# Kernel tuning notes

Measured on AMD Instinct MI355X. Metric: run time of the kernel, lower is better.

The kernel has to match this reference:

```python
import jax, jax.numpy as jnp
import numpy as np

B, T, E, H = 8, 2048, 512, 16
D = E // H  # 32 embeddings per head
LN_EPS = 1e-3  # keras LayerNormalization default epsilon
DECAY = 1.2


def setup_inputs() -> dict:
    key = jax.random.key(0)
    k0, k1, k2 = jax.random.split(key, 3)
    x = jax.random.normal(k0, (B, T, E), dtype=jnp.float32)
    W = jax.random.normal(k1, (E, E), dtype=jnp.float32) * (1.0 / np.sqrt(E))
    b = jnp.zeros((E,), dtype=jnp.float32)
    concept_map = jax.random.normal(k2, (H, D, D, D), dtype=jnp.float32) * 0.02
    gamma = jnp.ones((E,), dtype=jnp.float32)
    beta = jnp.zeros((E,), dtype=jnp.float32)
    return {"x": x, "W": W, "b": b, "concept_map": concept_map,
            "gamma": gamma, "beta": beta}


def reference(x, W, b, concept_map, gamma, beta):
    Bn, Tn, En = x.shape
    Hn = concept_map.shape[0]
    Dn = En // Hn
    # Dense projection, split into heads: (B,T,H,D)
    h = (jnp.einsum('bte,ef->btf', x, W) + b).reshape(Bn, Tn, Hn, Dn)
    # Decayed cumulative sum of preceding tokens: S_0 = 0, S_t = (S_{t-1} + h_{t-1}) / 1.2
    def step(s, h_t):
        return (s + h_t) / DECAY, s
    _, S = jax.lax.scan(step, jnp.zeros((Bn, Hn, Dn), h.dtype),
                        jnp.swapaxes(h, 0, 1))  # S: (T,B,H,D)
    S = jnp.swapaxes(S, 0, 1)  # (B,T,H,D)
    # Fused bilinear contraction: sum_{i,j} h[...,i] * S[...,j] * C[h,k,i,j]
    # (equivalent to outer-product * concept_map then reduce_sum over last two dims)
    y = jnp.einsum('bthi,bthj,hkij->bthk', h, S, concept_map) + h
    y = y.reshape(Bn, Tn, En)
    # LayerNormalization over last axis (keras default eps=1e-3)
    mu = jnp.mean(y, axis=-1, keepdims=True)
    var = jnp.var(y, axis=-1, keepdims=True)
    y = (y - mu) * jax.lax.rsqrt(var + LN_EPS) * gamma + beta
    # Dropout: identity at inference
    return y
```

## Files before the change

### kernel.cpp

```cpp
#include <hip/hip_runtime.h>
#include <hip/hip_bf16.h>

#define Bn 8
#define Tn 2048
#define En 512
#define Hn 16
#define Dn 32
#define NC 32
#define CL 64
#define NT (Bn*Tn)
#define INV_DECAY (1.0f/1.2f)

typedef __attribute__((ext_vector_type(8))) short  bf16x8;
typedef __attribute__((ext_vector_type(4))) float  f32x4;
typedef __attribute__((ext_vector_type(8))) unsigned short u16x8;

__device__ __forceinline__ unsigned short f2b(float f) {
    __hip_bfloat16 h = __float2bfloat16(f);
    return *reinterpret_cast<unsigned short*>(&h);
}
__device__ __forceinline__ float b2f(unsigned short u) {
    union { unsigned int i; float f; } c; c.i = ((unsigned int)u) << 16; return c.f;
}

__device__ __forceinline__ size_t hm(int hd, int tok, int ch) {
    return (size_t)hd * ((size_t)NT * Dn) + (size_t)tok * Dn + ch;
}

__global__ __launch_bounds__(256) void prep_k(const float* __restrict__ C,
                                              unsigned short* __restrict__ Cl,
                                              const float* __restrict__ W,
                                              unsigned short* __restrict__ Wt) {
    __shared__ float tile[32][33];
    if (blockIdx.x < 256) {
        const int g = blockIdx.x * 256 + threadIdx.x;
        const int hd = g >> 12, rem = g & 4095;
        const int i = rem >> 7, half = (rem >> 6) & 1, lane = rem & 63;
        const int tloc = lane & 15, kgrp = lane >> 4;
        const int k = half * 16 + tloc;
        const float* src = C + (size_t)hd * 32768 + (size_t)k * 1024 + i * 32 + kgrp * 8;
        float4 a = reinterpret_cast<const float4*>(src)[0];
        float4 b = reinterpret_cast<const float4*>(src)[1];
        u16x8 st;
        st[0]=f2b(a.x); st[1]=f2b(a.y); st[2]=f2b(a.z); st[3]=f2b(a.w);
        st[4]=f2b(b.x); st[5]=f2b(b.y); st[6]=f2b(b.z); st[7]=f2b(b.w);
        *reinterpret_cast<u16x8*>(Cl + (size_t)g * 8) = st;
    } else {
        const int bid = blockIdx.x - 256;
        const int kb = (bid & 15) * 32, nb = (bid >> 4) * 32;
        const int tx = threadIdx.x & 31, ty = threadIdx.x >> 5;
        #pragma unroll
        for (int j = 0; j < 4; j++)
            tile[ty + 8 * j][tx] = W[(size_t)(kb + ty + 8 * j) * En + nb + tx];
        __syncthreads();
        #pragma unroll
        for (int j = 0; j < 4; j++)
            Wt[(size_t)(nb + ty + 8 * j) * En + kb + tx] = f2b(tile[tx][ty + 8 * j]);
    }
}

__global__ __launch_bounds__(256) void gemm_mfma_k(const float* __restrict__ x,
                                                   const unsigned short* __restrict__ Wt,
                                                   const float* __restrict__ bias,
                                                   unsigned short* __restrict__ h) {
    __shared__ unsigned short As[128][40];
    __shared__ unsigned short Bs[64][40];
    const int m0 = blockIdx.x * 128, n0 = blockIdx.y * 64;
    const int tid = threadIdx.x;
    const int wid = tid >> 6, lane = tid & 63;
    const int tloc = lane & 15, kgrp = lane >> 4;
    const int wr = wid >> 1, wc = wid & 1;

    const int ar = tid >> 1, ah = (tid & 1) * 16;
    const int brr = tid >> 2, bq = (tid & 3) * 8;

    f32x4 acc[4][2] = {};

    for (int k0 = 0; k0 < En; k0 += 32) {
        const float* xp = &x[(size_t)(m0 + ar) * En + k0 + ah];
        float4 a0 = reinterpret_cast<const float4*>(xp)[0];
        float4 a1 = reinterpret_cast<const float4*>(xp)[1];
        float4 a2 = reinterpret_cast<const float4*>(xp)[2];
        float4 a3 = reinterpret_cast<const float4*>(xp)[3];
        u16x8 bv = *reinterpret_cast<const u16x8*>(&Wt[(size_t)(n0 + brr) * En + k0 + bq]);
        __syncthreads();
        u16x8 w0, w1;
        w0[0]=f2b(a0.x); w0[1]=f2b(a0.y); w0[2]=f2b(a0.z); w0[3]=f2b(a0.w);
        w0[4]=f2b(a1.x); w0[5]=f2b(a1.y); w0[6]=f2b(a1.z); w0[7]=f2b(a1.w);
        w1[0]=f2b(a2.x); w1[1]=f2b(a2.y); w1[2]=f2b(a2.z); w1[3]=f2b(a2.w);
        w1[4]=f2b(a3.x); w1[5]=f2b(a3.y); w1[6]=f2b(a3.z); w1[7]=f2b(a3.w);
        *reinterpret_cast<u16x8*>(&As[ar][ah])     = w0;
        *reinterpret_cast<u16x8*>(&As[ar][ah + 8]) = w1;
        *reinterpret_cast<u16x8*>(&Bs[brr][bq])    = bv;
        __syncthreads();

        bf16x8 afr[4], bfr[2];
        #pragma unroll
        for (int m = 0; m < 4; m++)
            afr[m] = *reinterpret_cast<const bf16x8*>(&As[wr * 64 + m * 16 + tloc][kgrp * 8]);
        #pragma unroll
        for (int n = 0; n < 2; n++)
            bfr[n] = *reinterpret_cast<const bf16x8*>(&Bs[wc * 32 + n * 16 + tloc][kgrp * 8]);
        #pragma unroll
        for (int m = 0; m < 4; m++)
            #pragma unroll
            for (int n = 0; n < 2; n++)
                acc[m][n] = __builtin_amdgcn_mfma_f32_16x16x32_bf16(afr[m], bfr[n], acc[m][n], 0, 0, 0);
    }

    #pragma unroll
    for (int n = 0; n < 2; n++) {
        const int col = n0 + wc * 32 + n * 16 + tloc;
        const float bcol = bias[col];
        const int hd = col >> 5, ch = col & 31;
        #pragma unroll
        for (int m = 0; m < 4; m++)
            #pragma unroll
            for (int r = 0; r < 4; r++) {
                const int row = m0 + wr * 64 + m * 16 + kgrp * 4 + r;
                h[hm(hd, row, ch)] = f2b(acc[m][n][r] + bcol);
            }
    }
}

__global__ __launch_bounds__(512) void scan_local_k(const unsigned short* __restrict__ h,
                                                    float* __restrict__ locals) {
    const int c = blockIdx.x, b = blockIdx.y;
    const int e = threadIdx.x;
    const int hd = e >> 5, ch = e & 31;
    const unsigned short* hp = h + hm(hd, b * Tn + c * CL, ch);
    float s = 0.f;
    for (int t = 0; t < CL; t++) s = (s + b2f(hp[(size_t)t * Dn])) * INV_DECAY;
    locals[(size_t)(b * NC + c) * En + e] = s;
}

__global__ __launch_bounds__(512) void scan_prefix_k(const float* __restrict__ locals,
                                                     float* __restrict__ Acar) {
    const int b = blockIdx.x;
    const int e = threadIdx.x;
    float invRL = 1.f;
    #pragma unroll
    for (int i = 0; i < CL; i++) invRL *= INV_DECAY;
    float A = 0.f;
    for (int c = 0; c < NC; c++) {
        Acar[(size_t)(b * NC + c) * En + e] = A;
        A = A * invRL + locals[(size_t)(b * NC + c) * En + e];
    }
}

__global__ __launch_bounds__(512) void scan_emit_k(const unsigned short* __restrict__ h,
                                                   const float* __restrict__ Acar,
                                                   unsigned short* __restrict__ Sg) {
    const int c = blockIdx.x, b = blockIdx.y;
    const int e = threadIdx.x;
    const int hd = e >> 5, ch = e & 31;
    float s = Acar[(size_t)(b * NC + c) * En + e];
    const size_t base = hm(hd, b * Tn + c * CL, ch);
    for (int t = 0; t < CL; t++) {
        Sg[base + (size_t)t * Dn] = f2b(s);
        s = (s + b2f(h[base + (size_t)t * Dn])) * INV_DECAY;
    }
}

__global__ __launch_bounds__(256) void bilinear7_k(const unsigned short* __restrict__ hg,
                                                   unsigned short* __restrict__ Sio,
                                                   const unsigned short* __restrict__ Cl) {
    __shared__ float ys[4][64][34];

    const int hd = blockIdx.y;
    const int tid = threadIdx.x;
    const int wid = tid >> 6, lane = tid & 63;
    const int tloc = lane & 15, kgrp = lane >> 4;
    const int j0 = kgrp * 8;
    const int tokens0 = blockIdx.x * 256 + wid * 64;

    u16x8 hreg[4][4];
    float sf[4][8];
    #pragma unroll
    for (int m = 0; m < 4; m++) {
        const int trow = tokens0 + m * 16 + tloc;
        const unsigned short* hrow = hg + hm(hd, trow, 0);
        #pragma unroll
        for (int q = 0; q < 4; q++)
            hreg[m][q] = *reinterpret_cast<const u16x8*>(hrow + q * 8);
        u16x8 sv = *reinterpret_cast<const u16x8*>(Sio + hm(hd, trow, j0));
        #pragma unroll
        for (int e = 0; e < 8; e++) sf[m][e] = b2f(sv[e]);
    }

    f32x4 acc[4][2] = {};
    const bf16x8* bb = reinterpret_cast<const bf16x8*>(Cl + (size_t)hd * 32768);

    #pragma unroll
    for (int i = 0; i < Dn; i++) {
        bf16x8 b0 = bb[i * 128 + lane];
        bf16x8 b1 = bb[i * 128 + 64 + lane];
        #pragma unroll
        for (int m = 0; m < 4; m++) {
            const float hsc = b2f(hreg[m][i >> 3][i & 7]);
            bf16x8 a;
            #pragma unroll
            for (int e = 0; e < 8; e++) a[e] = (short)f2b(hsc * sf[m][e]);
            acc[m][0] = __builtin_amdgcn_mfma_f32_16x16x32_bf16(a, b0, acc[m][0], 0, 0, 0);
            acc[m][1] = __builtin_amdgcn_mfma_f32_16x16x32_bf16(a, b1, acc[m][1], 0, 0, 0);
        }
    }

    #pragma unroll
    for (int m = 0; m < 4; m++)
        #pragma unroll
        for (int nt = 0; nt < 2; nt++)
            #pragma unroll
            for (int r = 0; r < 4; r++)
                ys[wid][m * 16 + kgrp * 4 + r][nt * 16 + tloc] = acc[m][nt][r];
    __syncthreads();

    {
        const float* yrow = &ys[wid][lane][0];
        const unsigned short* hrow = hg + hm(hd, tokens0 + lane, 0);
        unsigned short* orow = Sio + hm(hd, tokens0 + lane, 0);
        #pragma unroll
        for (int q = 0; q < 4; q++) {
            u16x8 hres = *reinterpret_cast<const u16x8*>(hrow + q * 8);
            u16x8 s;
            #pragma unroll
            for (int e2 = 0; e2 < 4; e2++) {
                float2 v = *reinterpret_cast<const float2*>(yrow + q * 8 + e2 * 2);
                s[e2 * 2]     = f2b(v.x + b2f(hres[e2 * 2]));
                s[e2 * 2 + 1] = f2b(v.y + b2f(hres[e2 * 2 + 1]));
            }
            *reinterpret_cast<u16x8*>(orow + q * 8) = s;
        }
    }
}

__global__ __launch_bounds__(256) void ln_k(const unsigned short* __restrict__ y,
                                            const float* __restrict__ gamma,
                                            const float* __restrict__ beta,
                                            float* __restrict__ out) {
    const int row = blockIdx.x * 4 + (threadIdx.x >> 6);
    const int lane = threadIdx.x & 63;
    u16x8 v = *reinterpret_cast<const u16x8*>(y + hm(lane >> 2, row, (lane & 3) * 8));
    float f[8];
    float s = 0.f, s2 = 0.f;
    #pragma unroll
    for (int e = 0; e < 8; e++) {
        f[e] = b2f(v[e]);
        s += f[e]; s2 += f[e] * f[e];
    }
    #pragma unroll
    for (int off = 1; off < 64; off <<= 1) {
        s  += __shfl_xor(s, off);
        s2 += __shfl_xor(s2, off);
    }
    const float mu = s * (1.f / En);
    const float var = s2 * (1.f / En) - mu * mu;
    const float rs = rsqrtf(var + 1e-3f);
    const int cbase = lane * 8;
    float4 g0 = reinterpret_cast<const float4*>(&gamma[cbase])[0];
    float4 g1 = reinterpret_cast<const float4*>(&gamma[cbase])[1];
    float4 b0 = reinterpret_cast<const float4*>(&beta[cbase])[0];
    float4 b1 = reinterpret_cast<const float4*>(&beta[cbase])[1];
    float4 o0, o1;
    o0.x = (f[0] - mu) * rs * g0.x + b0.x; o0.y = (f[1] - mu) * rs * g0.y + b0.y;
    o0.z = (f[2] - mu) * rs * g0.z + b0.z; o0.w = (f[3] - mu) * rs * g0.w + b0.w;
    o1.x = (f[4] - mu) * rs * g1.x + b1.x; o1.y = (f[5] - mu) * rs * g1.y + b1.y;
    o1.z = (f[6] - mu) * rs * g1.z + b1.z; o1.w = (f[7] - mu) * rs * g1.w + b1.w;
    float* op = out + (size_t)row * En;
    reinterpret_cast<float4*>(op)[lane * 2]     = o0;
    reinterpret_cast<float4*>(op)[lane * 2 + 1] = o1;
}

extern "C" void kernel_launch(void* const* d_in, const int* in_sizes, int n_in,
                              void* d_out, int out_size, void* d_ws, size_t ws_size,
                              hipStream_t stream) {
    const float* x     = (const float*)d_in[0];
    const float* W     = (const float*)d_in[1];
    const float* bias  = (const float*)d_in[2];
    const float* C     = (const float*)d_in[3];
    const float* gamma = (const float*)d_in[4];
    const float* beta  = (const float*)d_in[5];
    float* out = (float*)d_out;

    unsigned short* hb  = (unsigned short*)d_ws;
    unsigned short* Sg  = hb + (size_t)Hn * NT * Dn;
    unsigned short* Cl  = Sg + (size_t)Hn * NT * Dn;
    unsigned short* Wt  = Cl + (size_t)Hn * Dn * Dn * Dn;
    float* locals = (float*)(Wt + (size_t)En * En);
    float* Acar   = locals + (size_t)Bn * NC * En;

    prep_k<<<512, 256, 0, stream>>>(C, Cl, W, Wt);
    gemm_mfma_k<<<dim3(NT / 128, En / 64), 256, 0, stream>>>(x, Wt, bias, hb);
    scan_local_k<<<dim3(NC, Bn), 512, 0, stream>>>(hb, locals);
    scan_prefix_k<<<Bn, 512, 0, stream>>>(locals, Acar);
    scan_emit_k<<<dim3(NC, Bn), 512, 0, stream>>>(hb, Acar, Sg);
    bilinear7_k<<<dim3(NT / 256, Hn), 256, 0, stream>>>(hb, Sg, Cl);
    ln_k<<<NT / 4, 256, 0, stream>>>(Sg, gamma, beta, out);
}
```

Baseline: 91.37 us.

## Split bilinear contraction over i across waves with register-resident concept-map fragments

The bilinear kernel now gives each wave a quarter of the i dimension and keeps that slice of the concept map in registers as MFMA A operands, instead of streaming the whole concept map per wave for 64 tokens. Each block handles 64 tokens, and the four waves' partial sums are reduced through shared memory before the residual add and store. This cuts repeated global/L2 reads of the concept map and raises the block count. The cost is an extra cross-wave LDS reduction and more register pressure, with occupancy set via launch bounds of 3 blocks.

```diff
diff --git a/kernel.cpp b/kernel.cpp
--- a/kernel.cpp
+++ b/kernel.cpp
@@ -162,75 +162,80 @@
     }
 }
 
-__global__ __launch_bounds__(256) void bilinear7_k(const unsigned short* __restrict__ hg,
-                                                   unsigned short* __restrict__ Sio,
-                                                   const unsigned short* __restrict__ Cl) {
-    __shared__ float ys[4][64][34];
+__global__ __launch_bounds__(256, 3) void bilinear8_k(const unsigned short* __restrict__ hg,
+                                                      unsigned short* __restrict__ Sio,
+                                                      const unsigned short* __restrict__ Cl) {
+    __shared__ float ys[4][64][36];
 
     const int hd = blockIdx.y;
     const int tid = threadIdx.x;
     const int wid = tid >> 6, lane = tid & 63;
     const int tloc = lane & 15, kgrp = lane >> 4;
     const int j0 = kgrp * 8;
-    const int tokens0 = blockIdx.x * 256 + wid * 64;
-
-    u16x8 hreg[4][4];
+    const int tokens0 = blockIdx.x * 64;
+
+    bf16x8 afr[8][2];
+    {
+        const unsigned short* cb = Cl + (size_t)hd * 32768;
+        #pragma unroll
+        for (int s = 0; s < 8; s++) {
+            const int i = wid * 8 + s;
+            #pragma unroll
+            for (int mt = 0; mt < 2; mt++)
+                afr[s][mt] = *reinterpret_cast<const bf16x8*>(
+                    cb + ((size_t)((i * 2 + mt) * 64 + lane) * 8));
+        }
+    }
+
+    u16x8 hreg[4];
     float sf[4][8];
     #pragma unroll
-    for (int m = 0; m < 4; m++) {
-        const int trow = tokens0 + m * 16 + tloc;
-        const unsigned short* hrow = hg + hm(hd, trow, 0);
-        #pragma unroll
-        for (int q = 0; q < 4; q++)
-            hreg[m][q] = *reinterpret_cast<const u16x8*>(hrow + q * 8);
+    for (int nt = 0; nt < 4; nt++) {
+        const int trow = tokens0 + nt * 16 + tloc;
+        hreg[nt] = *reinterpret_cast<const u16x8*>(hg + hm(hd, trow, wid * 8));
         u16x8 sv = *reinterpret_cast<const u16x8*>(Sio + hm(hd, trow, j0));
         #pragma unroll
-        for (int e = 0; e < 8; e++) sf[m][e] = b2f(sv[e]);
-    }
-
-    f32x4 acc[4][2] = {};
-    const bf16x8* bb = reinterpret_cast<const bf16x8*>(Cl + (size_t)hd * 32768);
-
-    #pragma unroll
-    for (int i = 0; i < Dn; i++) {
-        bf16x8 b0 = bb[i * 128 + lane];
-        bf16x8 b1 = bb[i * 128 + 64 + lane];
-        #pragma unroll
-        for (int m = 0; m < 4; m++) {
-            const float hsc = b2f(hreg[m][i >> 3][i & 7]);
-            bf16x8 a;
-            #pragma unroll
-            for (int e = 0; e < 8; e++) a[e] = (short)f2b(hsc * sf[m][e]);
-            acc[m][0] = __builtin_amdgcn_mfma_f32_16x16x32_bf16(a, b0, acc[m][0], 0, 0, 0);
-            acc[m][1] = __builtin_amdgcn_mfma_f32_16x16x32_bf16(a, b1, acc[m][1], 0, 0, 0);
+        for (int e = 0; e < 8; e++) sf[nt][e] = b2f(sv[e]);
+    }
+
+    f32x4 acc[2][4] = {};
+    #pragma unroll
+    for (int s = 0; s < 8; s++) {
+        #pragma unroll
+        for (int nt = 0; nt < 4; nt++) {
+            const float hsc = b2f(hreg[nt][s]);
+            bf16x8 bfrag;
+            #pragma unroll
+            for (int e = 0; e < 8; e++) bfrag[e] = (short)f2b(hsc * sf[nt][e]);
+            acc[0][nt] = __builtin_amdgcn_mfma_f32_16x16x32_bf16(afr[s][0], bfrag, acc[0][nt], 0, 0, 0);
+            acc[1][nt] = __builtin_amdgcn_mfma_f32_16x16x32_bf16(afr[s][1], bfrag, acc[1][nt], 0, 0, 0);
         }
     }
 
     #pragma unroll
-    for (int m = 0; m < 4; m++)
-        #pragma unroll
-        for (int nt = 0; nt < 2; nt++)
-            #pragma unroll
-            for (int r = 0; r < 4; r++)
-                ys[wid][m * 16 + kgrp * 4 + r][nt * 16 + tloc] = acc[m][nt][r];
+    for (int mt = 0; mt < 2; mt++)
+        #pragma unroll
+        for (int nt = 0; nt < 4; nt++)
+            *reinterpret_cast<f32x4*>(&ys[wid][nt * 16 + tloc][mt * 16 + kgrp * 4]) = acc[mt][nt];
     __syncthreads();
 
     {
-        const float* yrow = &ys[wid][lane][0];
-        const unsigned short* hrow = hg + hm(hd, tokens0 + lane, 0);
-        unsigned short* orow = Sio + hm(hd, tokens0 + lane, 0);
-        #pragma unroll
-        for (int q = 0; q < 4; q++) {
-            u16x8 hres = *reinterpret_cast<const u16x8*>(hrow + q * 8);
-            u16x8 s;
-            #pragma unroll
-            for (int e2 = 0; e2 < 4; e2++) {
-                float2 v = *reinterpret_cast<const float2*>(yrow + q * 8 + e2 * 2);
-                s[e2 * 2]     = f2b(v.x + b2f(hres[e2 * 2]));
-                s[e2 * 2 + 1] = f2b(v.y + b2f(hres[e2 * 2 + 1]));
-            }
-            *reinterpret_cast<u16x8*>(orow + q * 8) = s;
+        const int token = tid >> 2, q = tid & 3;
+        float y[8];
+        #pragma unroll
+        for (int e = 0; e < 8; e++) y[e] = 0.f;
+        #pragma unroll
+        for (int w = 0; w < 4; w++) {
+            const float* src = &ys[w][token][q * 8];
+            #pragma unroll
+            for (int e = 0; e < 8; e++) y[e] += src[e];
         }
+        const unsigned short* hrow = hg + hm(hd, tokens0 + token, q * 8);
+        u16x8 hres = *reinterpret_cast<const u16x8*>(hrow);
+        u16x8 st;
+        #pragma unroll
+        for (int e = 0; e < 8; e++) st[e] = f2b(y[e] + b2f(hres[e]));
+        *reinterpret_cast<u16x8*>(Sio + hm(hd, tokens0 + token, q * 8)) = st;
     }
 }
 
@@ -294,6 +299,6 @@
     scan_local_k<<<dim3(NC, Bn), 512, 0, stream>>>(hb, locals);
     scan_prefix_k<<<Bn, 512, 0, stream>>>(locals, Acar);
     scan_emit_k<<<dim3(NC, Bn), 512, 0, stream>>>(hb, Acar, Sg);
-    bilinear7_k<<<dim3(NT / 256, Hn), 256, 0, stream>>>(hb, Sg, Cl);
+    bilinear8_k<<<dim3(NT / 64, Hn), 256, 0, stream>>>(hb, Sg, Cl);
     ln_k<<<NT / 4, 256, 0, stream>>>(Sg, gamma, beta, out);
 }
```

Result: faster. 83.55 us (-8.6%).
